# Kernel optimization log

Hardware: AMD Instinct MI355X
Metric: run time of the kernel (lower is better)

The kernel has to match this reference:

```python
import jax, jax.numpy as jnp
import numpy as np

# irreps kept in the output (sorted): 0e (dim 1), 1o (dim 3), 2e (dim 5)
IRS = (("0e", 1), ("1o", 3), ("2e", 5))
# multiplicity of each irrep in the reduced symmetric tensor product basis per order
MULS = {1: {"0e": 1, "1o": 1, "2e": 1},
        2: {"0e": 2, "1o": 2, "2e": 3},
        3: {"0e": 4, "1o": 6, "2e": 8}}
N, C, D, S, CORR = 1024, 128, 9, 10, 3  # nodes, channels, irreps dim (0e+1o+2e), species, correlation


def setup_inputs() -> dict:
    key = jax.random.key(0)
    ks = iter(jax.random.split(key, 64))
    inp = {"x": jax.random.normal(next(ks), (N, C, D), dtype=jnp.float32)}
    for order in range(1, CORR + 1):
        for ir, idim in IRS:
            mul = MULS[order][ir]
            # U basis tensor: shape (D,)*order + (mul, ir_dim); CG-like tensors are sparse
            u = jax.random.normal(next(ks), (D,) * order + (mul, idim), dtype=jnp.float32)
            mask = jax.random.bernoulli(next(ks), 0.25, u.shape)
            inp[f"u{order}_{ir}"] = jnp.where(mask, u, 0.0)
            # per-species weights, stddev mul**-0.5 ('element' gradient normalization)
            inp[f"w{order}_{ir}"] = jax.random.normal(next(ks), (S, mul, C), dtype=jnp.float32) * (mul ** -0.5)
    inp["index"] = jax.random.randint(next(ks), (N,), 0, S)
    return inp


def _forward(x, index, us, ws):
    # x: (N, C, D) node features; index: (N,) species ids
    out = {}
    for order in range(CORR, 0, -1):
        for ir, idim in IRS:
            w = ws[order][ir][index]  # per-species weight gather -> (N, mul, C)
            u = us[order][ir]          # (D,)*order + (mul, idim)
            if order == CORR:
                # highest order: contract one D axis with x together with the weights
                out[ir] = jnp.einsum('...jki,zkc,zcj->zc...i', u, w, x)
            else:
                # accumulate this order's term, then contract one more D axis with x
                acc = out[ir] + jnp.einsum('...ki,zkc->zc...i', u, w)
                out[ir] = jnp.einsum('zc...ji,zcj->zc...i', acc, x)
    # final out[ir]: (N, C, idim); axis_to_mul -> concat of (N, C*idim) blocks
    return jnp.concatenate([out[ir].reshape(N, C * idim) for ir, idim in IRS], axis=-1)


def reference(x, u1_0e, u1_1o, u1_2e, u2_0e, u2_1o, u2_2e, u3_0e, u3_1o, u3_2e,
              w1_0e, w1_1o, w1_2e, w2_0e, w2_1o, w2_2e, w3_0e, w3_1o, w3_2e, index):
    us = {1: {"0e": u1_0e, "1o": u1_1o, "2e": u1_2e},
          2: {"0e": u2_0e, "1o": u2_1o, "2e": u2_2e},
          3: {"0e": u3_0e, "1o": u3_1o, "2e": u3_2e}}
    ws = {1: {"0e": w1_0e, "1o": w1_1o, "2e": w1_2e},
          2: {"0e": w2_0e, "1o": w2_1o, "2e": w2_2e},
          3: {"0e": w3_0e, "1o": w3_1o, "2e": w3_2e}}
    return _forward(x, index, us, ws)
```

## Files before the change

kernel.cpp:

```cpp
#include <hip/hip_runtime.h>


#define NMONO 219
#define NN 1024
#define NC 128
#define NS 10
#define NPB 4
#define PADBLK 272
#define FOLD_CHUNK 16
#define NCHUNKF ((NMONO + FOLD_CHUNK - 1) / FOLD_CHUNK)

struct Tables { int mt[NMONO]; };

constexpr Tables make_tables() {
    Tables T{};
    int m = 0;
    for (int a = 0; a < 9; a++)
        for (int b = a; b < 10; b++)
            for (int j = b; j < 10; j++) { T.mt[m] = (a << 8) | (b << 4) | j; m++; }
    return T;
}
__device__ __constant__ const Tables TBL = make_tables();

__global__ __launch_bounds__(64) void usym_build(
    const float* __restrict__ u1_0e, const float* __restrict__ u1_1o, const float* __restrict__ u1_2e,
    const float* __restrict__ u2_0e, const float* __restrict__ u2_1o, const float* __restrict__ u2_2e,
    const float* __restrict__ u3_0e, const float* __restrict__ u3_1o, const float* __restrict__ u3_2e,
    const int* __restrict__ index,
    float* __restrict__ usumAll,
    int* __restrict__ perm, int* __restrict__ offs, int* __restrict__ blockmap)
{
    const int t = threadIdx.x;

    if (blockIdx.x == NMONO) {
        __shared__ int cnt[NS], pos[NS], nbstart[NS+1];
        __shared__ int sh_nch;
        if (t < NS) cnt[t] = 0;
        __syncthreads();
        for (int n = t; n < NN; n += 64) atomicAdd(&cnt[index[n]], 1);
        __syncthreads();
        if (t == 0) {
            int o = 0, g = 0;
            for (int i = 0; i < NS; i++) {
                offs[i] = o; pos[i] = o; o += cnt[i];
                nbstart[i] = g; g += (cnt[i] + NPB - 1) / NPB;
            }
            offs[NS] = o; nbstart[NS] = g; sh_nch = g;
        }
        __syncthreads();
        const int Nch = sh_nch;
        for (int p = t; p < PADBLK; p += 64) { blockmap[2*p] = -1; blockmap[2*p+1] = 0; }
        __syncthreads();
        for (int g = t; g < Nch; g += 64) {
            const int q = Nch >> 3, r = Nch & 7;
            int x = 0, stx = 0;
            for (int xx = 0; xx < 8; xx++) {
                const int cx = q + (xx < r ? 1 : 0);
                if (g < stx + cx) { x = xx; break; }
                stx += cx;
            }
            const int p = x + 8 * (g - stx);
            int sp = 0;
            while (g >= nbstart[sp+1]) sp++;
            blockmap[2*p]   = sp;
            blockmap[2*p+1] = g - nbstart[sp];
        }
        for (int n = t; n < NN; n += 64) {
            const int s = index[n];
            const int r = atomicAdd(&pos[s], 1);
            perm[r] = n;
        }
        return;
    }

    const int m = blockIdx.x;
    const int e = TBL.mt[m];
    const int A = (e >> 8) & 15, B = (e >> 4) & 15, J = e & 15;
    float sv = 0.f;
    if (J < 9) {
        if (t < 62) {
            const float* u; int mul, idim, k, i;
            if (t < 4)       { u = u3_0e; mul = 4; idim = 1; k = t; i = 0; }
            else if (t < 22) { u = u3_1o; mul = 6; idim = 3; int r = t - 4;  k = r / 3; i = r % 3; }
            else             { u = u3_2e; mul = 8; idim = 5; int r = t - 22; k = r / 5; i = r % 5; }
            int arr[6] = { A*81+B*9+J, A*81+J*9+B, B*81+A*9+J, B*81+J*9+A, J*81+A*9+B, J*81+B*9+A };
            for (int p = 0; p < 6; p++) {
                bool dup = false;
                for (int q = 0; q < p; q++) if (arr[q] == arr[p]) dup = true;
                if (!dup) sv += u[arr[p]*(mul*idim) + k*idim + i];
            }
        }
    } else if (B < 9) {
        if (t < 23) {
            const float* u; int mul, idim, k, i;
            if (t < 2)      { u = u2_0e; mul = 2; idim = 1; k = t; i = 0; }
            else if (t < 8) { u = u2_1o; mul = 2; idim = 3; int r = t - 2; k = r / 3; i = r % 3; }
            else            { u = u2_2e; mul = 3; idim = 5; int r = t - 8; k = r / 5; i = r % 5; }
            sv = u[(A*9+B)*(mul*idim) + k*idim + i];
            if (A != B) sv += u[(B*9+A)*(mul*idim) + k*idim + i];
        }
    } else {
        if (t < 9) {
            if (t == 0)      sv = u1_0e[A];
            else if (t < 4)  sv = u1_1o[A*3 + (t-1)];
            else             sv = u1_2e[A*5 + (t-4)];
        }
    }
    usumAll[m*64 + t] = sv;
}

__global__ __launch_bounds__(128) void uw_fold(
    const float* __restrict__ w1_0e, const float* __restrict__ w1_1o, const float* __restrict__ w1_2e,
    const float* __restrict__ w2_0e, const float* __restrict__ w2_1o, const float* __restrict__ w2_2e,
    const float* __restrict__ w3_0e, const float* __restrict__ w3_1o, const float* __restrict__ w3_2e,
    const float* __restrict__ usumAll,
    float* __restrict__ uwA, float* __restrict__ uwB)
{
    const int s  = blockIdx.x / NCHUNKF;
    const int m0 = (blockIdx.x % NCHUNKF) * FOLD_CHUNK;
    const int c  = threadIdx.x;
    __shared__ float us[FOLD_CHUNK][64];

    for (int f = c; f < FOLD_CHUNK*64; f += 128) {
        const int mm = f >> 6, sl = f & 63, m = m0 + mm;
        us[mm][sl] = (m < NMONO) ? usumAll[m*64 + sl] : 0.f;
    }
    __syncthreads();

    float W30[4], W31[6], W32[8], W20[2], W21[2], W22[3];
    #pragma unroll
    for (int k = 0; k < 4; k++) W30[k] = w3_0e[(s*4+k)*NC + c];
    #pragma unroll
    for (int k = 0; k < 6; k++) W31[k] = w3_1o[(s*6+k)*NC + c];
    #pragma unroll
    for (int k = 0; k < 8; k++) W32[k] = w3_2e[(s*8+k)*NC + c];
    #pragma unroll
    for (int k = 0; k < 2; k++) W20[k] = w2_0e[(s*2+k)*NC + c];
    #pragma unroll
    for (int k = 0; k < 2; k++) W21[k] = w2_1o[(s*2+k)*NC + c];
    #pragma unroll
    for (int k = 0; k < 3; k++) W22[k] = w2_2e[(s*3+k)*NC + c];
    const float W10 = w1_0e[s*NC + c], W11 = w1_1o[s*NC + c], W12 = w1_2e[s*NC + c];

    for (int mm = 0; mm < FOLD_CHUNK; mm++) {
        const int m = m0 + mm;
        if (m >= NMONO) break;
        const int e = TBL.mt[m];
        const int B = (e >> 4) & 15, J = e & 15;
        float o[9];
        if (J < 9) {
            float v = 0.f;
            #pragma unroll
            for (int k = 0; k < 4; k++) v += us[mm][k] * W30[k];
            o[0] = v;
            #pragma unroll
            for (int i = 0; i < 3; i++) {
                v = 0.f;
                #pragma unroll
                for (int k = 0; k < 6; k++) v += us[mm][4 + k*3 + i] * W31[k];
                o[1+i] = v;
            }
            #pragma unroll
            for (int i = 0; i < 5; i++) {
                v = 0.f;
                #pragma unroll
                for (int k = 0; k < 8; k++) v += us[mm][22 + k*5 + i] * W32[k];
                o[4+i] = v;
            }
        } else if (B < 9) {
            float v = 0.f;
            #pragma unroll
            for (int k = 0; k < 2; k++) v += us[mm][k] * W20[k];
            o[0] = v;
            #pragma unroll
            for (int i = 0; i < 3; i++) {
                v = 0.f;
                #pragma unroll
                for (int k = 0; k < 2; k++) v += us[mm][2 + k*3 + i] * W21[k];
                o[1+i] = v;
            }
            #pragma unroll
            for (int i = 0; i < 5; i++) {
                v = 0.f;
                #pragma unroll
                for (int k = 0; k < 3; k++) v += us[mm][8 + k*5 + i] * W22[k];
                o[4+i] = v;
            }
        } else {
            o[0] = us[mm][0] * W10;
            #pragma unroll
            for (int i = 0; i < 3; i++) o[1+i] = us[mm][1+i] * W11;
            #pragma unroll
            for (int i = 0; i < 5; i++) o[4+i] = us[mm][4+i] * W12;
        }
        const size_t base = (size_t)(s*NMONO + m)*NC + c;
        float4 lo; lo.x = o[0]; lo.y = o[1]; lo.z = o[2]; lo.w = o[3];
        float4 hi; hi.x = o[4]; hi.y = o[5]; hi.z = o[6]; hi.w = o[7];
        *(float4*)(uwA + base*8)     = lo;
        *(float4*)(uwA + base*8 + 4) = hi;
        uwB[base] = o[8];
    }
}

#define FMA_NODE(Q, P, F0, F1, FB)                                          \
    acc[Q][0] += F0.x*(P); acc[Q][1] += F0.y*(P); acc[Q][2] += F0.z*(P);    \
    acc[Q][3] += F0.w*(P); acc[Q][4] += F1.x*(P); acc[Q][5] += F1.y*(P);    \
    acc[Q][6] += F1.z*(P); acc[Q][7] += F1.w*(P); acc[Q][8] += FB*(P);

#define CONSUME(MM, F0, F1, FB)                                             \
    { const int e = TBL.mt[MM];                                             \
      const float4 xa = *(const float4*)&lx4[c44 + ((e>>8)&15)*4];          \
      const float4 xb = *(const float4*)&lx4[c44 + ((e>>4)&15)*4];          \
      const float4 xj = *(const float4*)&lx4[c44 + (e&15)*4];               \
      FMA_NODE(0, xa.x*xb.x*xj.x, F0, F1, FB)                               \
      FMA_NODE(1, xa.y*xb.y*xj.y, F0, F1, FB)                               \
      FMA_NODE(2, xa.z*xb.z*xj.z, F0, F1, FB)                               \
      FMA_NODE(3, xa.w*xb.w*xj.w, F0, F1, FB) }

#define RED_WRITE(SLOT)                                                     \
    { float* r = &red[SLOT][c][0];                                          \
      _Pragma("unroll")                                                     \
      for (int q = 0; q < 4; q++)                                           \
          _Pragma("unroll")                                                 \
          for (int i = 0; i < 9; i++) r[q*9 + i] = acc[q][i]; }

#define RED_ADD(SLOT)                                                       \
    { const float* r = &red[SLOT][c][0];                                    \
      _Pragma("unroll")                                                     \
      for (int q = 0; q < 4; q++)                                           \
          _Pragma("unroll")                                                 \
          for (int i = 0; i < 9; i++) acc[q][i] += r[q*9 + i]; }

__global__ __launch_bounds__(512, 4) void symcon_main(
    const float* __restrict__ x,
    const int* __restrict__ perm, const int* __restrict__ offs,
    const int* __restrict__ blockmap,
    const float* __restrict__ uwA, const float* __restrict__ uwB,
    float* __restrict__ out)
{
    __shared__ __align__(16) float lx4[128 * 44];
    __shared__ float red[2][128][36];

    const int tid = threadIdx.x;
    const int z   = tid >> 7;
    const int c   = tid & 127;
    const int c44 = c * 44;

    const int s     = blockmap[2*blockIdx.x];
    const int chunk = blockmap[2*blockIdx.x + 1];
    if (s < 0) return;
    const int gbeg = offs[s], gend = offs[s+1];
    const int p0   = gbeg + chunk*NPB;

    int node[4]; bool valid[4];
    #pragma unroll
    for (int q = 0; q < 4; q++) {
        const int pi = p0 + q;
        valid[q] = (pi < gend);
        node[q]  = perm[valid[q] ? pi : p0];
    }

    #pragma unroll
    for (int q = 0; q < 4; q++) {
        const size_t nb = (size_t)node[q] * 1152;
        for (int f = tid; f < 1152; f += 512) {
            const int ch = f / 9, d = f - ch*9;
            lx4[ch*44 + d*4 + q] = x[nb + f];
        }
    }
    { const int ch = tid >> 2, q = tid & 3; lx4[ch*44 + 36 + q] = 1.0f; }
    __syncthreads();

    float acc[4][9];
    #pragma unroll
    for (int q = 0; q < 4; q++)
        #pragma unroll
        for (int i = 0; i < 9; i++) acc[q][i] = 0.f;

    const int mbeg = 55 * z;
    const int mend = (z == 3) ? NMONO : mbeg + 55;

    const float* pa = uwA + ((size_t)(s*NMONO + mbeg)*NC + c) * 8;
    const float* pb = uwB +  (size_t)(s*NMONO + mbeg)*NC + c;

    float4 A0 = *(const float4*)pa, A1 = *(const float4*)(pa + 4); float Ab = *pb;
    float4 B0 = *(const float4*)(pa + NC*8), B1 = *(const float4*)(pa + NC*8 + 4); float Bb = *(pb + NC);

    for (int m = mbeg; m < mend; m += 2) {
        const bool h2 = (m + 2 < mend), h3 = (m + 3 < mend);
        const float* ra = h2 ? pa + 2*NC*8 : pa;
        const float* rb = h2 ? pb + 2*NC   : pb;
        const float* sa = h3 ? pa + 3*NC*8 : pa;
        const float* sb = h3 ? pb + 3*NC   : pb;
        const float4 nA0 = *(const float4*)ra, nA1 = *(const float4*)(ra + 4); const float nAb = *rb;
        const float4 nB0 = *(const float4*)sa, nB1 = *(const float4*)(sa + 4); const float nBb = *sb;
        CONSUME(m, A0, A1, Ab)
        if (m + 1 < mend) { CONSUME(m + 1, B0, B1, Bb) }
        A0 = nA0; A1 = nA1; Ab = nAb;
        B0 = nB0; B1 = nB1; Bb = nBb;
        pa += 2*NC*8; pb += 2*NC;
    }

    if (z == 2 || z == 3) RED_WRITE(z - 2)
    __syncthreads();
    if (z == 0 || z == 1) RED_ADD(z)
    __syncthreads();
    if (z == 1) RED_WRITE(0)
    __syncthreads();
    if (z == 0) {
        RED_ADD(0)
        #pragma unroll
        for (int q = 0; q < 4; q++) {
            if (!valid[q]) continue;
            float* orow = out + (size_t)node[q] * 1152;
            orow[c] = acc[q][0];
            #pragma unroll
            for (int i = 0; i < 3; i++) orow[128 + c*3 + i] = acc[q][1+i];
            #pragma unroll
            for (int i = 0; i < 5; i++) orow[512 + c*5 + i] = acc[q][4+i];
        }
    }
}

extern "C" void kernel_launch(void* const* d_in, const int* in_sizes, int n_in,
                              void* d_out, int out_size, void* d_ws, size_t ws_size,
                              hipStream_t stream)
{
    const float* x     = (const float*)d_in[0];
    const float* u1_0e = (const float*)d_in[1];
    const float* w1_0e = (const float*)d_in[2];
    const float* u1_1o = (const float*)d_in[3];
    const float* w1_1o = (const float*)d_in[4];
    const float* u1_2e = (const float*)d_in[5];
    const float* w1_2e = (const float*)d_in[6];
    const float* u2_0e = (const float*)d_in[7];
    const float* w2_0e = (const float*)d_in[8];
    const float* u2_1o = (const float*)d_in[9];
    const float* w2_1o = (const float*)d_in[10];
    const float* u2_2e = (const float*)d_in[11];
    const float* w2_2e = (const float*)d_in[12];
    const float* u3_0e = (const float*)d_in[13];
    const float* w3_0e = (const float*)d_in[14];
    const float* u3_1o = (const float*)d_in[15];
    const float* w3_1o = (const float*)d_in[16];
    const float* u3_2e = (const float*)d_in[17];
    const float* w3_2e = (const float*)d_in[18];
    const int*   index = (const int*)d_in[19];
    float* out = (float*)d_out;

    float* uwA     = (float*)d_ws;
    float* uwB     = uwA + (size_t)NS*NMONO*NC*8;
    float* usumAll = uwB + (size_t)NS*NMONO*NC;
    int*   perm     = (int*)(usumAll + NMONO*64);
    int*   offs     = perm + NN;
    int*   blockmap = offs + (NS+1);

    hipLaunchKernelGGL(usym_build, dim3(NMONO + 1), dim3(64), 0, stream,
        u1_0e, u1_1o, u1_2e, u2_0e, u2_1o, u2_2e, u3_0e, u3_1o, u3_2e,
        index, usumAll, perm, offs, blockmap);

    hipLaunchKernelGGL(uw_fold, dim3(NS*NCHUNKF), dim3(128), 0, stream,
        w1_0e, w1_1o, w1_2e, w2_0e, w2_1o, w2_2e, w3_0e, w3_1o, w3_2e,
        usumAll, uwA, uwB);

    hipLaunchKernelGGL(symcon_main, dim3(PADBLK), dim3(512), 0, stream,
        x, perm, offs, blockmap, uwA, uwB, out);
}
```

Measured before the change: 153.6 us.

## Split monomial loop across eight waves per block with 1024-thread blocks

Doubles the block to 1024 threads so eight channel-groups each handle about 28 monomials instead of four groups with 55. The manual double-buffered prefetch of folded weights is replaced by a simple unroll-2 loop. The cross-group reduction gains extra shared-memory rounds and barriers. The intent is to shorten each thread's serial FMA chain and add latency-hiding parallelism, at the cost of more syncs and possibly tighter register limits from launch bounds (1024, 8).

```diff
diff --git a/kernel.cpp b/kernel.cpp
--- a/kernel.cpp
+++ b/kernel.cpp
@@ -207,16 +207,6 @@
     acc[Q][3] += F0.w*(P); acc[Q][4] += F1.x*(P); acc[Q][5] += F1.y*(P);    \
     acc[Q][6] += F1.z*(P); acc[Q][7] += F1.w*(P); acc[Q][8] += FB*(P);
 
-#define CONSUME(MM, F0, F1, FB)                                             \
-    { const int e = TBL.mt[MM];                                             \
-      const float4 xa = *(const float4*)&lx4[c44 + ((e>>8)&15)*4];          \
-      const float4 xb = *(const float4*)&lx4[c44 + ((e>>4)&15)*4];          \
-      const float4 xj = *(const float4*)&lx4[c44 + (e&15)*4];               \
-      FMA_NODE(0, xa.x*xb.x*xj.x, F0, F1, FB)                               \
-      FMA_NODE(1, xa.y*xb.y*xj.y, F0, F1, FB)                               \
-      FMA_NODE(2, xa.z*xb.z*xj.z, F0, F1, FB)                               \
-      FMA_NODE(3, xa.w*xb.w*xj.w, F0, F1, FB) }
-
 #define RED_WRITE(SLOT)                                                     \
     { float* r = &red[SLOT][c][0];                                          \
       _Pragma("unroll")                                                     \
@@ -231,7 +221,7 @@
           _Pragma("unroll")                                                 \
           for (int i = 0; i < 9; i++) acc[q][i] += r[q*9 + i]; }
 
-__global__ __launch_bounds__(512, 4) void symcon_main(
+__global__ __launch_bounds__(1024, 8) void symcon_main(
     const float* __restrict__ x,
     const int* __restrict__ perm, const int* __restrict__ offs,
     const int* __restrict__ blockmap,
@@ -263,12 +253,12 @@
     #pragma unroll
     for (int q = 0; q < 4; q++) {
         const size_t nb = (size_t)node[q] * 1152;
-        for (int f = tid; f < 1152; f += 512) {
+        for (int f = tid; f < 1152; f += 1024) {
             const int ch = f / 9, d = f - ch*9;
             lx4[ch*44 + d*4 + q] = x[nb + f];
         }
     }
-    { const int ch = tid >> 2, q = tid & 3; lx4[ch*44 + 36 + q] = 1.0f; }
+    if (tid < 512) { const int ch = tid >> 2, q = tid & 3; lx4[ch*44 + 36 + q] = 1.0f; }
     __syncthreads();
 
     float acc[4][9];
@@ -277,31 +267,37 @@
         #pragma unroll
         for (int i = 0; i < 9; i++) acc[q][i] = 0.f;
 
-    const int mbeg = 55 * z;
-    const int mend = (z == 3) ? NMONO : mbeg + 55;
+    const int mbeg = (z < 3) ? 28*z : 84 + 27*(z - 3);
+    const int mend = mbeg + ((z < 3) ? 28 : 27);
 
     const float* pa = uwA + ((size_t)(s*NMONO + mbeg)*NC + c) * 8;
     const float* pb = uwB +  (size_t)(s*NMONO + mbeg)*NC + c;
 
-    float4 A0 = *(const float4*)pa, A1 = *(const float4*)(pa + 4); float Ab = *pb;
-    float4 B0 = *(const float4*)(pa + NC*8), B1 = *(const float4*)(pa + NC*8 + 4); float Bb = *(pb + NC);
-
-    for (int m = mbeg; m < mend; m += 2) {
-        const bool h2 = (m + 2 < mend), h3 = (m + 3 < mend);
-        const float* ra = h2 ? pa + 2*NC*8 : pa;
-        const float* rb = h2 ? pb + 2*NC   : pb;
-        const float* sa = h3 ? pa + 3*NC*8 : pa;
-        const float* sb = h3 ? pb + 3*NC   : pb;
-        const float4 nA0 = *(const float4*)ra, nA1 = *(const float4*)(ra + 4); const float nAb = *rb;
-        const float4 nB0 = *(const float4*)sa, nB1 = *(const float4*)(sa + 4); const float nBb = *sb;
-        CONSUME(m, A0, A1, Ab)
-        if (m + 1 < mend) { CONSUME(m + 1, B0, B1, Bb) }
-        A0 = nA0; A1 = nA1; Ab = nAb;
-        B0 = nB0; B1 = nB1; Bb = nBb;
-        pa += 2*NC*8; pb += 2*NC;
+    #pragma unroll 2
+    for (int m = mbeg; m < mend; ++m) {
+        const int e = TBL.mt[m];
+        const float4 xa = *(const float4*)&lx4[c44 + ((e>>8)&15)*4];
+        const float4 xb = *(const float4*)&lx4[c44 + ((e>>4)&15)*4];
+        const float4 xj = *(const float4*)&lx4[c44 + (e&15)*4];
+        const float4 f0 = *(const float4*)(pa);
+        const float4 f1 = *(const float4*)(pa + 4);
+        const float  fb = *pb;
+        FMA_NODE(0, xa.x*xb.x*xj.x, f0, f1, fb)
+        FMA_NODE(1, xa.y*xb.y*xj.y, f0, f1, fb)
+        FMA_NODE(2, xa.z*xb.z*xj.z, f0, f1, fb)
+        FMA_NODE(3, xa.w*xb.w*xj.w, f0, f1, fb)
+        pa += NC*8; pb += NC;
     }
 
     if (z == 2 || z == 3) RED_WRITE(z - 2)
+    __syncthreads();
+    if (z == 0 || z == 1) RED_ADD(z)
+    __syncthreads();
+    if (z == 6 || z == 7) RED_WRITE(z - 6)
+    __syncthreads();
+    if (z == 4 || z == 5) RED_ADD(z - 4)
+    __syncthreads();
+    if (z == 4 || z == 5) RED_WRITE(z - 4)
     __syncthreads();
     if (z == 0 || z == 1) RED_ADD(z)
     __syncthreads();
@@ -363,6 +359,6 @@
         w1_0e, w1_1o, w1_2e, w2_0e, w2_1o, w2_2e, w3_0e, w3_1o, w3_2e,
         usumAll, uwA, uwB);
 
-    hipLaunchKernelGGL(symcon_main, dim3(PADBLK), dim3(512), 0, stream,
+    hipLaunchKernelGGL(symcon_main, dim3(PADBLK), dim3(1024), 0, stream,
         x, perm, offs, blockmap, uwA, uwB, out);
 }
```

After: 210.9 us. 37.3% more time.
